# Performance work log

Hardware: AMD Instinct MI355X
Metric: run time of the kernel (lower is better)

## Reference

```python
import jax, jax.numpy as jnp
import numpy as np

B = 8192        # batch
F = 16          # num_fields
V = 50000       # vocab per field
D = 32          # embed_dim (all equal per assert)
NE = 3          # number of embedding spaces
NL = 3          # cross-net layers
EOD = F * D     # 512 = embed_output_dim
M1, M2, M3 = 512, 256, 128
REG_WEIGHT = 0.01


def setup_inputs() -> dict:
    key = jax.random.key(0)
    ks = jax.random.split(key, 12)
    x = jax.random.randint(ks[0], (B, F), 0, V)
    emb_tables = jax.random.normal(ks[1], (NE, F * V, D), dtype=jnp.float32) * 0.05
    cross_W = jax.random.normal(ks[2], (NE, NL, EOD, EOD), dtype=jnp.float32) * (1.0 / np.sqrt(EOD))
    cross_b = jnp.zeros((NE, NL, EOD), dtype=jnp.float32)
    mlp1_W = jax.random.normal(ks[3], (NE, EOD, M1), dtype=jnp.float32) * (1.0 / np.sqrt(EOD))
    mlp1_b = jnp.zeros((NE, M1), dtype=jnp.float32)
    mlp_W1 = jax.random.normal(ks[4], (M1, M2), dtype=jnp.float32) * (1.0 / np.sqrt(M1))
    mlp_b1 = jnp.zeros((M2,), dtype=jnp.float32)
    mlp_W2 = jax.random.normal(ks[5], (M2, M3), dtype=jnp.float32) * (1.0 / np.sqrt(M2))
    mlp_b2 = jnp.zeros((M3,), dtype=jnp.float32)
    mlp_W3 = jax.random.normal(ks[6], (M3, 1), dtype=jnp.float32) * (1.0 / np.sqrt(M3))
    mlp_b3 = jnp.zeros((1,), dtype=jnp.float32)
    return {"x": x, "emb_tables": emb_tables, "cross_W": cross_W, "cross_b": cross_b,
            "mlp1_W": mlp1_W, "mlp1_b": mlp1_b, "mlp_W1": mlp_W1, "mlp_b1": mlp_b1,
            "mlp_W2": mlp_W2, "mlp_b2": mlp_b2, "mlp_W3": mlp_W3, "mlp_b3": mlp_b3}


def _branch(x0, Ws, bs, W1, b1):
    # DCNv2 cross network: x_{l+1} = x0 * (W_l x_l + b_l) + x_l, then one MLP layer (ReLU)
    xl = x0
    for l in range(NL):
        xl = x0 * (xl @ Ws[l] + bs[l]) + xl
    return jax.nn.relu(xl @ W1 + b1)


def reference(x, emb_tables, cross_W, cross_b, mlp1_W, mlp1_b,
              mlp_W1, mlp_b1, mlp_W2, mlp_b2, mlp_W3, mlp_b3):
    offsets = jnp.arange(F, dtype=x.dtype) * V
    idx = x + offsets                      # [B, F] indices into shared table
    es = emb_tables[:, idx]                # [NE, B, F, D]
    es_flat = es.reshape(NE, B, EOD)       # [NE, B, F*D]
    h = jax.vmap(_branch)(es_flat, cross_W, cross_b, mlp1_W, mlp1_b)  # [NE, B, M1]
    h = h.mean(axis=0)                     # mean over embedding spaces
    h = jax.nn.relu(h @ mlp_W1 + mlp_b1)
    h = jax.nn.relu(h @ mlp_W2 + mlp_b2)
    p = h @ mlp_W3 + mlp_b3                # [B, 1]
    output = jax.nn.sigmoid(p[:, 0])
    # training-path regularizer: per-field cross-embedding Gram SVDs
    pairs = [(1, 0), (2, 0), (2, 1)]
    sims = []
    for i, j in pairs:
        m = jnp.einsum('bkd,bke->kde', es[i], es[j])     # [F, D, D]
        s = jnp.linalg.svd(m, compute_uv=False)          # batched singular values [F, D]
        sims.append(s.mean(axis=0))                      # [D]
    sim = jnp.concatenate(sims)                          # [len(pairs)*D]
    reg_loss = REG_WEIGHT * jnp.mean(sim ** 2)
    return output, reg_loss
```

## Files before the change

### kernel.cpp

```cpp
#include <hip/hip_runtime.h>
#include <math.h>

#define B_ 8192
#define F_ 16
#define V_ 50000
#define D_ 32
#define NE_ 3
#define EOD_ 512
#define M1_ 512
#define M2_ 256
#define M3_ 128
#define BE_ ((size_t)B_ * EOD_)

typedef __attribute__((ext_vector_type(8))) short short8;
typedef __attribute__((ext_vector_type(4))) float floatx4;

__device__ __forceinline__ unsigned short f2bf(float f) {
    union { float f; unsigned u; } v; v.f = f;
    unsigned r = v.u + 0x7FFF + ((v.u >> 16) & 1);
    return (unsigned short)(r >> 16);
}
__device__ __forceinline__ float bf2f(unsigned short h) {
    union { unsigned u; float f; } v; v.u = (unsigned)h << 16;
    return v.f;
}
__device__ __forceinline__ void gld16(const void* g, void* l) {
    __builtin_amdgcn_global_load_lds(
        (const __attribute__((address_space(1))) unsigned int*)g,
        (__attribute__((address_space(3))) unsigned int*)l, 16, 0, 0);
}

__global__ __launch_bounds__(256) void gather_k(const int* __restrict__ x,
    const float* __restrict__ tables, unsigned short* __restrict__ esb)
{
    int gid = blockIdx.x * 256 + threadIdx.x;
    int d8 = gid & 3;
    int f  = (gid >> 2) & 15;
    int b  = (gid >> 6) & (B_ - 1);
    int e  = gid >> 19;
    int idx = x[b * F_ + f] + f * V_;
    const float4* src = (const float4*)(tables + ((size_t)e * F_ * V_ + idx) * D_) + d8 * 2;
    float4 v0 = src[0], v1 = src[1];
    unsigned short o[8];
    o[0] = f2bf(v0.x); o[1] = f2bf(v0.y); o[2] = f2bf(v0.z); o[3] = f2bf(v0.w);
    o[4] = f2bf(v1.x); o[5] = f2bf(v1.y); o[6] = f2bf(v1.z); o[7] = f2bf(v1.w);
    unsigned short* dst = esb + ((size_t)e * B_ + b) * EOD_ + f * D_ + d8 * 8;
    *(uint4*)dst = *(uint4*)o;
}

__global__ __launch_bounds__(256) void wtrans_k(const float* __restrict__ W,
    unsigned short* __restrict__ Wt, int K, int N)
{
    __shared__ float tile[32][33];
    int bn = blockIdx.x * 32, bk = blockIdx.y * 32;
    int mat = blockIdx.z;
    const float* Wm = W + (size_t)mat * K * N;
    unsigned short* Wtm = Wt + (size_t)mat * K * N;
    int tx = threadIdx.x & 31, ty = threadIdx.x >> 5;
    #pragma unroll
    for (int i = 0; i < 32; i += 8)
        tile[ty + i][tx] = Wm[(size_t)(bk + ty + i) * N + bn + tx];
    __syncthreads();
    #pragma unroll
    for (int i = 0; i < 32; i += 8)
        Wtm[(size_t)(bn + ty + i) * K + bk + tx] = f2bf(tile[tx][ty + i]);
}

__global__ __launch_bounds__(256) void gemm_mfma_k(
    const unsigned short* __restrict__ A,  long sA,
    const unsigned short* __restrict__ Wt, long sW,
    const float* __restrict__ bias,        long sB,
    const unsigned short* __restrict__ x0, long sX,
    const unsigned short* __restrict__ xl, long sXl,
    unsigned short* __restrict__ outb,     long sO,
    int M, int N, int K, int mode)
{
    int e = blockIdx.z;
    A    += (size_t)e * sA;
    Wt   += (size_t)e * sW;
    bias += (size_t)e * sB;
    outb += (size_t)e * sO;
    if (mode == 0) { x0 += (size_t)e * sX; xl += (size_t)e * sXl; }

    __shared__ unsigned short As[128 * 32];
    __shared__ unsigned short Bs[128 * 32];
    int t = threadIdx.x;
    int w = t >> 6, lane = t & 63;
    int quad = lane >> 4, lid = lane & 15;
    int wr = (w & 1) * 64, wc = (w >> 1) * 64;
    int rowbase = blockIdx.y * 128, colbase = blockIdx.x * 128;

    int chunk = w * 2;
    int sub = lane >> 2;
    int kk = (lane & 3) * 8;
    const unsigned short* pa0 = A  + (size_t)(rowbase + chunk * 16 + sub) * K + kk;
    const unsigned short* pa1 = pa0 + (size_t)16 * K;
    const unsigned short* pb0 = Wt + (size_t)(colbase + chunk * 16 + sub) * K + kk;
    const unsigned short* pb1 = pb0 + (size_t)16 * K;
    unsigned short* la0 = As + chunk * 512 + lane * 8;
    unsigned short* la1 = la0 + 512;
    unsigned short* lb0 = Bs + chunk * 512 + lane * 8;
    unsigned short* lb1 = lb0 + 512;

    floatx4 acc[4][4];
    #pragma unroll
    for (int i = 0; i < 4; i++)
        #pragma unroll
        for (int j = 0; j < 4; j++) acc[i][j] = {0.f, 0.f, 0.f, 0.f};

    for (int k0 = 0; k0 < K; k0 += 32) {
        if (k0) __syncthreads();
        gld16(pa0 + k0, la0);
        gld16(pa1 + k0, la1);
        gld16(pb0 + k0, lb0);
        gld16(pb1 + k0, lb1);
        __syncthreads();
        short8 af[4], bfr[4];
        #pragma unroll
        for (int i = 0; i < 4; i++) {
            af[i]  = *(const short8*)(As + (wr + i * 16 + lid) * 32 + quad * 8);
            bfr[i] = *(const short8*)(Bs + (wc + i * 16 + lid) * 32 + quad * 8);
        }
        #pragma unroll
        for (int i = 0; i < 4; i++)
            #pragma unroll
            for (int j = 0; j < 4; j++)
                acc[i][j] = __builtin_amdgcn_mfma_f32_16x16x32_bf16(af[i], bfr[j], acc[i][j], 0, 0, 0);
    }

    #pragma unroll
    for (int i = 0; i < 4; i++) {
        int row0 = rowbase + wr + i * 16 + quad * 4;
        #pragma unroll
        for (int j = 0; j < 4; j++) {
            int col = colbase + wc + j * 16 + lid;
            float bv = bias[col];
            #pragma unroll
            for (int rr = 0; rr < 4; rr++) {
                size_t off = (size_t)(row0 + rr) * N + col;
                float v = acc[i][j][rr] + bv;
                if (mode == 0)      v = bf2f(x0[off]) * v + bf2f(xl[off]);
                else if (mode == 1) v = fmaxf(v, 0.f) * (1.f / 3.f);
                else                v = fmaxf(v, 0.f);
                outb[off] = f2bf(v);
            }
        }
    }
}

__global__ __launch_bounds__(256) void sum3_k(const unsigned short* __restrict__ h,
                                              unsigned short* __restrict__ o)
{
    size_t i = ((size_t)blockIdx.x * 256 + threadIdx.x) * 8;
    uint4 a = *(const uint4*)(h + i);
    uint4 b = *(const uint4*)(h + BE_ + i);
    uint4 c = *(const uint4*)(h + 2 * BE_ + i);
    const unsigned short* pa = (const unsigned short*)&a;
    const unsigned short* pb = (const unsigned short*)&b;
    const unsigned short* pc = (const unsigned short*)&c;
    unsigned short r[8];
    #pragma unroll
    for (int j = 0; j < 8; j++) r[j] = f2bf(bf2f(pa[j]) + bf2f(pb[j]) + bf2f(pc[j]));
    *(uint4*)(o + i) = *(uint4*)r;
}

__global__ __launch_bounds__(256) void final_k(const unsigned short* __restrict__ h2,
    const float* __restrict__ W3, const float* __restrict__ b3,
    float* __restrict__ out)
{
    int gt = blockIdx.x * 256 + threadIdx.x;
    int s = gt >> 6, lane = gt & 63;
    float p = bf2f(h2[(size_t)s * 128 + lane]) * W3[lane]
            + bf2f(h2[(size_t)s * 128 + 64 + lane]) * W3[64 + lane];
    #pragma unroll
    for (int off = 32; off > 0; off >>= 1) p += __shfl_down(p, off);
    if (lane == 0) out[s] = 1.0f / (1.0f + expf(-(p + b3[0])));
}

__global__ __launch_bounds__(256) void pairsum_k(const unsigned short* __restrict__ es,
                                                 float* __restrict__ m)
{
    const int pi[3] = {1, 2, 2};
    const int pj[3] = {0, 0, 1};
    int pk = blockIdx.x;
    int pair = pk >> 4, k = pk & 15;
    const unsigned short* Ei = es + (size_t)pi[pair] * BE_ + k * D_;
    const unsigned short* Ej = es + (size_t)pj[pair] * BE_ + k * D_;
    int b0 = blockIdx.y * (B_ / 16);

    __shared__ float sa[8][32], sb[8][32];
    int t = threadIdx.x;
    int d = t >> 3, e4 = (t & 7) * 4;
    int lr = t >> 5, lc = t & 31;
    float a0 = 0, a1 = 0, a2 = 0, a3 = 0;

    for (int bb = b0; bb < b0 + B_ / 16; bb += 8) {
        __syncthreads();
        sa[lr][lc] = bf2f(Ei[(size_t)(bb + lr) * EOD_ + lc]);
        sb[lr][lc] = bf2f(Ej[(size_t)(bb + lr) * EOD_ + lc]);
        __syncthreads();
        #pragma unroll
        for (int s2 = 0; s2 < 8; s2++) {
            float avv = sa[s2][d];
            float4 bvv = *(const float4*)&sb[s2][e4];
            a0 += avv * bvv.x; a1 += avv * bvv.y;
            a2 += avv * bvv.z; a3 += avv * bvv.w;
        }
    }
    float* dst = m + (size_t)pk * 1024 + d * 32 + e4;
    atomicAdd(dst + 0, a0); atomicAdd(dst + 1, a1);
    atomicAdd(dst + 2, a2); atomicAdd(dst + 3, a3);
}

__global__ __launch_bounds__(256) void svd_k(const float* __restrict__ mg,
                                             float* __restrict__ sv)
{
    __shared__ float Mm[4][32][32];
    __shared__ float G[4][32][33];
    __shared__ float rc[4][16], rs[4][16];
    int t = threadIdx.x;
    int w = t >> 6, l = t & 63;
    int mat = blockIdx.x * 4 + w;
    float (*Gm)[33] = G[w];
    float (*Mw)[32] = Mm[w];

    const float* src = mg + (size_t)mat * 1024;
    for (int u = l; u < 1024; u += 64) Mw[u >> 5][u & 31] = src[u];
    for (int u = l; u < 1024; u += 64) {
        int p = u >> 5, q = u & 31;
        float s = 0;
        #pragma unroll
        for (int dd = 0; dd < 32; dd++) s += Mw[dd][p] * Mw[dd][q];
        Gm[p][q] = s;
    }

    int colr = l & 31, half = l >> 5;
    for (int sweep = 0; sweep < 6; sweep++) {
        for (int r = 0; r < 31; r++) {
            if (l < 16) {
                int p, q;
                if (l == 0) { p = 31; q = r; }
                else { p = (r + l) % 31; q = (r + 31 - l) % 31; }
                float app = Gm[p][p], aqq = Gm[q][q], apq = Gm[p][q];
                float c = 1.f, s = 0.f;
                if (fabsf(apq) > 1e-12f) {
                    float tau = (aqq - app) / (2.f * apq);
                    float tt = (tau >= 0.f) ? 1.f / (tau + sqrtf(1.f + tau * tau))
                                            : 1.f / (tau - sqrtf(1.f + tau * tau));
                    c = rsqrtf(1.f + tt * tt); s = tt * c;
                }
                rc[w][l] = c; rs[w][l] = s;
            }
            int ps[8], qs[8];
            float cc[8], ssv[8], gp[8], gq[8];
            #pragma unroll
            for (int j = 0; j < 8; j++) {
                int pi_ = half + 2 * j;
                int p, q;
                if (pi_ == 0) { p = 31; q = r; }
                else { p = (r + pi_) % 31; q = (r + 31 - pi_) % 31; }
                ps[j] = p; qs[j] = q;
                cc[j] = rc[w][pi_]; ssv[j] = rs[w][pi_];
                gp[j] = Gm[p][colr]; gq[j] = Gm[q][colr];
            }
            #pragma unroll
            for (int j = 0; j < 8; j++) {
                Gm[ps[j]][colr] = cc[j] * gp[j] - ssv[j] * gq[j];
                Gm[qs[j]][colr] = ssv[j] * gp[j] + cc[j] * gq[j];
            }
            #pragma unroll
            for (int j = 0; j < 8; j++) {
                gp[j] = Gm[colr][ps[j]];
                gq[j] = Gm[colr][qs[j]];
            }
            #pragma unroll
            for (int j = 0; j < 8; j++) {
                Gm[colr][ps[j]] = cc[j] * gp[j] - ssv[j] * gq[j];
                Gm[colr][qs[j]] = ssv[j] * gp[j] + cc[j] * gq[j];
            }
        }
    }

    if (l < 32) Mw[0][l] = sqrtf(fmaxf(Gm[l][l], 0.f));
    if (l < 32) {
        float v = Mw[0][l];
        int rank = 0;
        for (int o2 = 0; o2 < 32; o2++) {
            float u2 = Mw[0][o2];
            if (u2 > v || (u2 == v && o2 < l)) rank++;
        }
        sv[(size_t)mat * 32 + rank] = v;
    }
}

__global__ __launch_bounds__(128) void reg_k(const float* __restrict__ sv,
                                             float* __restrict__ out)
{
    __shared__ float red[128];
    int t = threadIdx.x;
    float val = 0.f;
    if (t < 96) {
        int p = t >> 5, d = t & 31;
        float s = 0;
        #pragma unroll
        for (int k = 0; k < 16; k++) s += sv[(size_t)(p * 16 + k) * 32 + d];
        s *= (1.f / 16.f);
        val = s * s;
    }
    red[t] = val; __syncthreads();
    for (int off = 64; off > 0; off >>= 1) {
        if (t < off) red[t] += red[t + off];
        __syncthreads();
    }
    if (t == 0) out[B_] = 0.01f * red[0] / 96.f;
}

extern "C" void kernel_launch(void* const* d_in, const int* in_sizes, int n_in,
                              void* d_out, int out_size, void* d_ws, size_t ws_size,
                              hipStream_t stream)
{
    const int*   x      = (const int*)d_in[0];
    const float* emb    = (const float*)d_in[1];
    const float* crossW = (const float*)d_in[2];
    const float* crossb = (const float*)d_in[3];
    const float* mlp1W  = (const float*)d_in[4];
    const float* mlp1b  = (const float*)d_in[5];
    const float* W1     = (const float*)d_in[6];
    const float* b1     = (const float*)d_in[7];
    const float* W2     = (const float*)d_in[8];
    const float* b2     = (const float*)d_in[9];
    const float* W3     = (const float*)d_in[10];
    const float* b3     = (const float*)d_in[11];
    float* out = (float*)d_out;

    unsigned char* wsb = (unsigned char*)d_ws;
    size_t o = 0;
    auto alloc = [&](size_t bytes) -> void* {
        void* p = wsb + o; o += (bytes + 255) & ~(size_t)255; return p;
    };
    unsigned short* esb  = (unsigned short*)alloc(3 * BE_ * 2);
    unsigned short* B0   = (unsigned short*)alloc(3 * BE_ * 2);
    unsigned short* B1   = (unsigned short*)alloc(3 * BE_ * 2);
    unsigned short* WtC  = (unsigned short*)alloc((size_t)9 * 512 * 512 * 2);
    unsigned short* WtM  = (unsigned short*)alloc((size_t)3 * 512 * 512 * 2);
    unsigned short* Wt1  = (unsigned short*)alloc((size_t)512 * 256 * 2);
    unsigned short* Wt2  = (unsigned short*)alloc((size_t)256 * 128 * 2);
    float*          mbuf = (float*)alloc(48 * 1024 * 4);
    float*          svb  = (float*)alloc(48 * 32 * 4);
    unsigned short* hsb = B0;
    unsigned short* h1b = B0 + (size_t)B_ * M1_;
    unsigned short* h2b = h1b + (size_t)B_ * M2_;

    wtrans_k<<<dim3(16, 16, 9), 256, 0, stream>>>(crossW, WtC, 512, 512);
    wtrans_k<<<dim3(16, 16, 3), 256, 0, stream>>>(mlp1W,  WtM, 512, 512);
    wtrans_k<<<dim3( 8, 16, 1), 256, 0, stream>>>(W1, Wt1, 512, 256);
    wtrans_k<<<dim3( 4,  8, 1), 256, 0, stream>>>(W2, Wt2, 256, 128);

    gather_k<<<(NE_ * B_ * F_ * 4) / 256, 256, 0, stream>>>(x, emb, esb);

    hipMemsetAsync(mbuf, 0, 48 * 1024 * 4, stream);
    pairsum_k<<<dim3(48, 16), 256, 0, stream>>>(esb, mbuf);
    svd_k<<<12, 256, 0, stream>>>(mbuf, svb);
    reg_k<<<1, 128, 0, stream>>>(svb, out);

    const long sW512 = 3 * 512 * 512;
    gemm_mfma_k<<<dim3(4, 64, 3), 256, 0, stream>>>(
        esb, (long)BE_, WtC, sW512, crossb, 3 * 512,
        esb, (long)BE_, esb, (long)BE_, B0, (long)BE_, B_, EOD_, EOD_, 0);
    gemm_mfma_k<<<dim3(4, 64, 3), 256, 0, stream>>>(
        B0, (long)BE_, WtC + 512 * 512, sW512, crossb + 512, 3 * 512,
        esb, (long)BE_, B0, (long)BE_, B1, (long)BE_, B_, EOD_, EOD_, 0);
    gemm_mfma_k<<<dim3(4, 64, 3), 256, 0, stream>>>(
        B1, (long)BE_, WtC + 2 * 512 * 512, sW512, crossb + 1024, 3 * 512,
        esb, (long)BE_, B1, (long)BE_, B0, (long)BE_, B_, EOD_, EOD_, 0);
    gemm_mfma_k<<<dim3(4, 64, 3), 256, 0, stream>>>(
        B0, (long)BE_, WtM, 512 * 512, mlp1b, 512,
        nullptr, 0, nullptr, 0, B1, (long)BE_, B_, M1_, EOD_, 1);
    sum3_k<<<(B_ * M1_) / (256 * 8), 256, 0, stream>>>(B1, hsb);
    gemm_mfma_k<<<dim3(2, 64, 1), 256, 0, stream>>>(
        hsb, 0, Wt1, 0, b1, 0, nullptr, 0, nullptr, 0,
        h1b, 0, B_, M2_, M1_, 2);
    gemm_mfma_k<<<dim3(1, 64, 1), 256, 0, stream>>>(
        h1b, 0, Wt2, 0, b2, 0, nullptr, 0, nullptr, 0,
        h2b, 0, B_, M3_, M2_, 2);
    final_k<<<(B_ * 64) / 256, 256, 0, stream>>>(h2b, W3, b3, out);
}
```

Before: 817.0 us.

## Replace two-sided Gram Jacobi SVD with register-resident one-sided Jacobi; merge weight transposes

The SVD kernel stops forming the 32x32 Gram matrix in shared memory and applying two-sided Jacobi rotations. Instead it runs one-sided (Hestenes) Jacobi on the matrix columns held in registers, one wavefront per matrix, exchanging partner columns with cross-lane shuffles and taking singular values as column norms. This is meant to remove the shared-memory traffic and barriers on the serial SVD critical path and to spread the work over 48 blocks instead of 12. The cross-layer and MLP1 weight transposes are also merged into one launch, which removes one kernel launch.

```diff
diff --git a/kernel.cpp b/kernel.cpp
--- a/kernel.cpp
+++ b/kernel.cpp
@@ -48,22 +48,38 @@
     *(uint4*)dst = *(uint4*)o;
 }
 
-__global__ __launch_bounds__(256) void wtrans_k(const float* __restrict__ W,
-    unsigned short* __restrict__ Wt, int K, int N)
+__global__ __launch_bounds__(256) void wtrans12_k(const float* __restrict__ crossW,
+    const float* __restrict__ mlp1W, unsigned short* __restrict__ Wt)
 {
     __shared__ float tile[32][33];
     int bn = blockIdx.x * 32, bk = blockIdx.y * 32;
     int mat = blockIdx.z;
-    const float* Wm = W + (size_t)mat * K * N;
-    unsigned short* Wtm = Wt + (size_t)mat * K * N;
+    const float* Wm = (mat < 9) ? crossW + (size_t)mat * 512 * 512
+                                : mlp1W + (size_t)(mat - 9) * 512 * 512;
+    unsigned short* Wtm = Wt + (size_t)mat * 512 * 512;
     int tx = threadIdx.x & 31, ty = threadIdx.x >> 5;
     #pragma unroll
     for (int i = 0; i < 32; i += 8)
-        tile[ty + i][tx] = Wm[(size_t)(bk + ty + i) * N + bn + tx];
+        tile[ty + i][tx] = Wm[(size_t)(bk + ty + i) * 512 + bn + tx];
     __syncthreads();
     #pragma unroll
     for (int i = 0; i < 32; i += 8)
-        Wtm[(size_t)(bn + ty + i) * K + bk + tx] = f2bf(tile[tx][ty + i]);
+        Wtm[(size_t)(bn + ty + i) * 512 + bk + tx] = f2bf(tile[tx][ty + i]);
+}
+
+__global__ __launch_bounds__(256) void wtrans_k(const float* __restrict__ W,
+    unsigned short* __restrict__ Wt, int K, int N)
+{
+    __shared__ float tile[32][33];
+    int bn = blockIdx.x * 32, bk = blockIdx.y * 32;
+    int tx = threadIdx.x & 31, ty = threadIdx.x >> 5;
+    #pragma unroll
+    for (int i = 0; i < 32; i += 8)
+        tile[ty + i][tx] = W[(size_t)(bk + ty + i) * N + bn + tx];
+    __syncthreads();
+    #pragma unroll
+    for (int i = 0; i < 32; i += 8)
+        Wt[(size_t)(bn + ty + i) * K + bk + tx] = f2bf(tile[tx][ty + i]);
 }
 
 __global__ __launch_bounds__(256) void gemm_mfma_k(
@@ -212,82 +228,72 @@
     atomicAdd(dst + 2, a2); atomicAdd(dst + 3, a3);
 }
 
-__global__ __launch_bounds__(256) void svd_k(const float* __restrict__ mg,
-                                             float* __restrict__ sv)
-{
-    __shared__ float Mm[4][32][32];
-    __shared__ float G[4][32][33];
-    __shared__ float rc[4][16], rs[4][16];
-    int t = threadIdx.x;
-    int w = t >> 6, l = t & 63;
-    int mat = blockIdx.x * 4 + w;
-    float (*Gm)[33] = G[w];
-    float (*Mw)[32] = Mm[w];
-
-    const float* src = mg + (size_t)mat * 1024;
-    for (int u = l; u < 1024; u += 64) Mw[u >> 5][u & 31] = src[u];
-    for (int u = l; u < 1024; u += 64) {
-        int p = u >> 5, q = u & 31;
-        float s = 0;
-        #pragma unroll
-        for (int dd = 0; dd < 32; dd++) s += Mw[dd][p] * Mw[dd][q];
-        Gm[p][q] = s;
-    }
-
-    int colr = l & 31, half = l >> 5;
+__global__ __launch_bounds__(64) void svd_k(const float* __restrict__ mg,
+                                            float* __restrict__ sv)
+{
+    int mat = blockIdx.x;
+    int l = threadIdx.x;
+    int col = l & 31, half = l >> 5;
+    const float* src = mg + (size_t)mat * 1024 + half * 16 * 32 + col;
+    float a[16];
+    #pragma unroll
+    for (int j = 0; j < 16; j++) a[j] = src[j * 32];
+
     for (int sweep = 0; sweep < 6; sweep++) {
         for (int r = 0; r < 31; r++) {
-            if (l < 16) {
-                int p, q;
-                if (l == 0) { p = 31; q = r; }
-                else { p = (r + l) % 31; q = (r + 31 - l) % 31; }
-                float app = Gm[p][p], aqq = Gm[q][q], apq = Gm[p][q];
-                float c = 1.f, s = 0.f;
-                if (fabsf(apq) > 1e-12f) {
-                    float tau = (aqq - app) / (2.f * apq);
-                    float tt = (tau >= 0.f) ? 1.f / (tau + sqrtf(1.f + tau * tau))
-                                            : 1.f / (tau - sqrtf(1.f + tau * tau));
-                    c = rsqrtf(1.f + tt * tt); s = tt * c;
+            int partner, isp;
+            if (col == 31) { partner = r; isp = 1; }
+            else {
+                int u = col - r; if (u < 0) u += 31;
+                if (u == 0) { partner = 31; isp = 0; }
+                else {
+                    int v = 2 * r - col; v %= 31; if (v < 0) v += 31;
+                    partner = v;
+                    isp = (u <= 15) ? 1 : 0;
                 }
-                rc[w][l] = c; rs[w][l] = s;
             }
-            int ps[8], qs[8];
-            float cc[8], ssv[8], gp[8], gq[8];
-            #pragma unroll
-            for (int j = 0; j < 8; j++) {
-                int pi_ = half + 2 * j;
-                int p, q;
-                if (pi_ == 0) { p = 31; q = r; }
-                else { p = (r + pi_) % 31; q = (r + 31 - pi_) % 31; }
-                ps[j] = p; qs[j] = q;
-                cc[j] = rc[w][pi_]; ssv[j] = rs[w][pi_];
-                gp[j] = Gm[p][colr]; gq[j] = Gm[q][colr];
+            int plane = half * 32 + partner;
+            float b[16];
+            #pragma unroll
+            for (int j = 0; j < 16; j++) b[j] = __shfl(a[j], plane, 64);
+            float own = 0.f, cross = 0.f, par = 0.f;
+            #pragma unroll
+            for (int j = 0; j < 16; j++) {
+                own   += a[j] * a[j];
+                cross += a[j] * b[j];
+                par   += b[j] * b[j];
             }
-            #pragma unroll
-            for (int j = 0; j < 8; j++) {
-                Gm[ps[j]][colr] = cc[j] * gp[j] - ssv[j] * gq[j];
-                Gm[qs[j]][colr] = ssv[j] * gp[j] + cc[j] * gq[j];
+            own   += __shfl_xor(own, 32);
+            cross += __shfl_xor(cross, 32);
+            par   += __shfl_xor(par, 32);
+            float app = isp ? own : par;
+            float aqq = isp ? par : own;
+            float c = 1.f, s = 0.f;
+            if (fabsf(cross) > 1e-12f) {
+                float tau = (aqq - app) / (2.f * cross);
+                float tt = (tau >= 0.f) ? 1.f / (tau + sqrtf(1.f + tau * tau))
+                                        : 1.f / (tau - sqrtf(1.f + tau * tau));
+                c = rsqrtf(1.f + tt * tt); s = tt * c;
             }
-            #pragma unroll
-            for (int j = 0; j < 8; j++) {
-                gp[j] = Gm[colr][ps[j]];
-                gq[j] = Gm[colr][qs[j]];
-            }
-            #pragma unroll
-            for (int j = 0; j < 8; j++) {
-                Gm[colr][ps[j]] = cc[j] * gp[j] - ssv[j] * gq[j];
-                Gm[colr][qs[j]] = ssv[j] * gp[j] + cc[j] * gq[j];
-            }
-        }
-    }
-
-    if (l < 32) Mw[0][l] = sqrtf(fmaxf(Gm[l][l], 0.f));
-    if (l < 32) {
-        float v = Mw[0][l];
+            float sgn = isp ? -s : s;
+            #pragma unroll
+            for (int j = 0; j < 16; j++) a[j] = c * a[j] + sgn * b[j];
+        }
+    }
+
+    float nn = 0.f;
+    #pragma unroll
+    for (int j = 0; j < 16; j++) nn += a[j] * a[j];
+    nn += __shfl_xor(nn, 32);
+    float v = sqrtf(nn);
+
+    __shared__ float ev[32];
+    if (half == 0) ev[col] = v;
+    if (half == 0) {
         int rank = 0;
         for (int o2 = 0; o2 < 32; o2++) {
-            float u2 = Mw[0][o2];
-            if (u2 > v || (u2 == v && o2 < l)) rank++;
+            float w = ev[o2];
+            if (w > v || (w == v && o2 < col)) rank++;
         }
         sv[(size_t)mat * 32 + rank] = v;
     }
@@ -341,26 +347,25 @@
     unsigned short* esb  = (unsigned short*)alloc(3 * BE_ * 2);
     unsigned short* B0   = (unsigned short*)alloc(3 * BE_ * 2);
     unsigned short* B1   = (unsigned short*)alloc(3 * BE_ * 2);
-    unsigned short* WtC  = (unsigned short*)alloc((size_t)9 * 512 * 512 * 2);
-    unsigned short* WtM  = (unsigned short*)alloc((size_t)3 * 512 * 512 * 2);
+    unsigned short* WtC  = (unsigned short*)alloc((size_t)12 * 512 * 512 * 2);
     unsigned short* Wt1  = (unsigned short*)alloc((size_t)512 * 256 * 2);
     unsigned short* Wt2  = (unsigned short*)alloc((size_t)256 * 128 * 2);
     float*          mbuf = (float*)alloc(48 * 1024 * 4);
     float*          svb  = (float*)alloc(48 * 32 * 4);
+    unsigned short* WtM  = WtC + (size_t)9 * 512 * 512;
     unsigned short* hsb = B0;
     unsigned short* h1b = B0 + (size_t)B_ * M1_;
     unsigned short* h2b = h1b + (size_t)B_ * M2_;
 
-    wtrans_k<<<dim3(16, 16, 9), 256, 0, stream>>>(crossW, WtC, 512, 512);
-    wtrans_k<<<dim3(16, 16, 3), 256, 0, stream>>>(mlp1W,  WtM, 512, 512);
-    wtrans_k<<<dim3( 8, 16, 1), 256, 0, stream>>>(W1, Wt1, 512, 256);
-    wtrans_k<<<dim3( 4,  8, 1), 256, 0, stream>>>(W2, Wt2, 256, 128);
+    wtrans12_k<<<dim3(16, 16, 12), 256, 0, stream>>>(crossW, mlp1W, WtC);
+    wtrans_k<<<dim3( 8, 16), 256, 0, stream>>>(W1, Wt1, 512, 256);
+    wtrans_k<<<dim3( 4,  8), 256, 0, stream>>>(W2, Wt2, 256, 128);
 
     gather_k<<<(NE_ * B_ * F_ * 4) / 256, 256, 0, stream>>>(x, emb, esb);
 
     hipMemsetAsync(mbuf, 0, 48 * 1024 * 4, stream);
     pairsum_k<<<dim3(48, 16), 256, 0, stream>>>(esb, mbuf);
-    svd_k<<<12, 256, 0, stream>>>(mbuf, svb);
+    svd_k<<<48, 64, 0, stream>>>(mbuf, svb);
     reg_k<<<1, 128, 0, stream>>>(svb, out);
 
     const long sW512 = 3 * 512 * 512;
```

New measurement: 704.0 us. -13.8%, faster.
